# Kernel optimization log

Measured on AMD Instinct MI355X. Metric: run time of the kernel, lower is better.

Reference implementation:

```python
import jax, jax.numpy as jnp
import numpy as np

N_NODES = 50000
N_GENES = 512
N_EDGES = 800000
NUM_ITERATIONS = 5
MAX_CAP = 128
NNZ_FRAC = 0.1  # fraction of initially observed (nonzero) entries


def setup_inputs() -> dict:
    key = jax.random.key(0)
    k1, k2, k3, k4, k5 = jax.random.split(key, 5)
    x = jax.random.normal(k1, (N_NODES, N_GENES), dtype=jnp.float32)
    observed = jax.random.uniform(k2, (N_NODES, N_GENES)) < NNZ_FRAC
    x = jnp.where(observed, x, 0.0)  # sparse expression matrix
    edge_index = jax.random.randint(k3, (2, N_EDGES), 0, N_NODES, dtype=jnp.int32)
    edge_weight = jax.random.uniform(k4, (N_EDGES,), dtype=jnp.float32)
    max_imputation_per_cell = jax.random.randint(k5, (N_NODES,), 0, MAX_CAP, dtype=jnp.int32)
    return {
        "x": x,
        "edge_weight": edge_weight,
        "edge_index": edge_index,
        "max_imputation_per_cell": max_imputation_per_cell,
    }


def reference(x, edge_weight, edge_index, max_imputation_per_cell):
    n_nodes, n_genes = x.shape
    row, col = edge_index[0], edge_index[1]  # adj[row, col] = w; spmm: out[row] += w * x[col]
    original_x = x
    existing = x != 0  # observed entries are always reset to original values
    cap = max_imputation_per_cell[:, None]  # [N,1]
    base_key = jax.random.key(42)

    def step(carry, it):
        x, imp = carry
        # sparse adjacency propagation (torch.sparse.mm(adj, x))
        xp = jax.ops.segment_sum(edge_weight[:, None] * x[col], row, num_segments=n_nodes)
        # masked imputation reset: keep original observed values
        x = jnp.where(existing, original_x, xp)
        newly = (x != 0) & (~existing) & (~imp)
        imp = imp | newly
        # capacity-limited random reset: keep a random subset of at most
        # max_imputation_per_cell imputed genes per cell, zero the excess
        scores = jax.random.uniform(jax.random.fold_in(base_key, it), x.shape)
        scores = jnp.where(imp, scores, 2.0)  # non-imputed sort last (uniform < 1)
        rank = jnp.argsort(jnp.argsort(scores, axis=1), axis=1)  # rank among imputed
        keep = rank < cap
        reset = imp & (~keep)
        x = jnp.where(reset, 0.0, x)
        imp = imp & keep
        return (x, imp), None

    init = (x, jnp.zeros((n_nodes, n_genes), dtype=bool))
    (x, _), _ = jax.lax.scan(step, init, jnp.arange(NUM_ITERATIONS))
    return x
```

## Files before the change

### kernel.cpp

```cpp
#include <hip/hip_runtime.h>
#include <stdint.h>

#define N_NODES   50000
#define N_GENES   512
#define N_EDGES   800000
#define N_ITERS   5

#define C_CHUNKS  250
#define CHUNK_E   3200
#define NSUB      (CHUNK_E / 64)

#define REC_DW     384
#define REC_BYTES  1536

#define RECS_BYTES (50000ull * REC_BYTES + 256ull)
#define IMP_BYTES  3200000ull
#define CNT_BYTES  200000ull
#define PTR_BYTES  200004ull
#define CCOL_BYTES 3200000ull
#define CW_BYTES   3200000ull
#define RND_BYTES  50048ull
#define BSUM_BYTES 1024ull
#define WS_NEEDED (RECS_BYTES + IMP_BYTES + CNT_BYTES + PTR_BYTES + CCOL_BYTES + CW_BYTES + 2ull * RND_BYTES + BSUM_BYTES)

__host__ __device__ __forceinline__ uint32_t rotl32(uint32_t x, int r) {
  return (x << r) | (x >> (32 - r));
}

__host__ __device__ __forceinline__ void threefry2x32(uint32_t k0, uint32_t k1,
                                                      uint32_t x0, uint32_t x1,
                                                      uint32_t& o0, uint32_t& o1) {
  uint32_t k2 = k0 ^ k1 ^ 0x1BD11BDAu;
  x0 += k0; x1 += k1;
  x0 += x1; x1 = rotl32(x1, 13) ^ x0;
  x0 += x1; x1 = rotl32(x1, 15) ^ x0;
  x0 += x1; x1 = rotl32(x1, 26) ^ x0;
  x0 += x1; x1 = rotl32(x1, 6)  ^ x0;
  x0 += k1; x1 += k2 + 1u;
  x0 += x1; x1 = rotl32(x1, 17) ^ x0;
  x0 += x1; x1 = rotl32(x1, 29) ^ x0;
  x0 += x1; x1 = rotl32(x1, 16) ^ x0;
  x0 += x1; x1 = rotl32(x1, 24) ^ x0;
  x0 += k2; x1 += k0 + 2u;
  x0 += x1; x1 = rotl32(x1, 13) ^ x0;
  x0 += x1; x1 = rotl32(x1, 15) ^ x0;
  x0 += x1; x1 = rotl32(x1, 26) ^ x0;
  x0 += x1; x1 = rotl32(x1, 6)  ^ x0;
  x0 += k0; x1 += k1 + 3u;
  x0 += x1; x1 = rotl32(x1, 17) ^ x0;
  x0 += x1; x1 = rotl32(x1, 29) ^ x0;
  x0 += x1; x1 = rotl32(x1, 16) ^ x0;
  x0 += x1; x1 = rotl32(x1, 24) ^ x0;
  x0 += k1; x1 += k2 + 4u;
  x0 += x1; x1 = rotl32(x1, 13) ^ x0;
  x0 += x1; x1 = rotl32(x1, 15) ^ x0;
  x0 += x1; x1 = rotl32(x1, 26) ^ x0;
  x0 += x1; x1 = rotl32(x1, 6)  ^ x0;
  x0 += k2; x1 += k0 + 5u;
  o0 = x0; o1 = x1;
}

__device__ __forceinline__ uint32_t jax_bits_part32(uint32_t k0, uint32_t k1, uint32_t j) {
  uint32_t o0, o1;
  threefry2x32(k0, k1, 0u, j, o0, o1);
  return o0 ^ o1;
}

__global__ void chunk_hist(const int* __restrict__ rows, int* __restrict__ hist) {
  int c = blockIdx.x;
  int base = c * CHUNK_E;
  int* h = hist + (size_t)c * N_NODES;
  for (int i = threadIdx.x; i < CHUNK_E; i += blockDim.x)
    atomicAdd(&h[rows[base + i]], 1);
}

__global__ void row_scan(int* __restrict__ hist, int* __restrict__ cnt) {
  int r = blockIdx.x * blockDim.x + threadIdx.x;
  if (r >= N_NODES) return;
  int run = 0;
  for (int c = 0; c < C_CHUNKS; ++c) {
    size_t idx = (size_t)c * N_NODES + r;
    int t = hist[idx];
    hist[idx] = run;
    run += t;
  }
  cnt[r] = run;
}

#define SCAN_NB ((N_NODES + 255) / 256)
__global__ void scan_blk(const int* __restrict__ cnt, int* __restrict__ bsum) {
  int b = blockIdx.x, t = threadIdx.x;
  int i = b * 256 + t;
  int v = (i < N_NODES) ? cnt[i] : 0;
  int s = v;
  #pragma unroll
  for (int off = 32; off > 0; off >>= 1) s += __shfl_xor(s, off, 64);
  __shared__ int wsum[4];
  if ((t & 63) == 0) wsum[t >> 6] = s;
  __syncthreads();
  if (t == 0) bsum[b] = wsum[0] + wsum[1] + wsum[2] + wsum[3];
}

__global__ void scan_top(int* __restrict__ bsum) {
  int t = threadIdx.x;
  int lane = t & 63, wv = t >> 6;
  int v = (t < SCAN_NB) ? bsum[t] : 0;
  int incl = v;
  #pragma unroll
  for (int off = 1; off < 64; off <<= 1) {
    int u = __shfl_up(incl, off, 64);
    if (lane >= off) incl += u;
  }
  __shared__ int wtot[4];
  if (lane == 63) wtot[wv] = incl;
  __syncthreads();
  int woff = 0;
  for (int k = 0; k < 4; ++k) if (k < wv) woff += wtot[k];
  if (t < SCAN_NB) bsum[t] = woff + incl - v;
}

__global__ void scan_apply(const int* __restrict__ cnt, const int* __restrict__ bbase,
                           int* __restrict__ ptr) {
  int b = blockIdx.x, t = threadIdx.x;
  int i = b * 256 + t;
  int lane = t & 63, wv = t >> 6;
  int v = (i < N_NODES) ? cnt[i] : 0;
  int incl = v;
  #pragma unroll
  for (int off = 1; off < 64; off <<= 1) {
    int u = __shfl_up(incl, off, 64);
    if (lane >= off) incl += u;
  }
  __shared__ int wtot[4];
  if (lane == 63) wtot[wv] = incl;
  __syncthreads();
  int woff = bbase[b];
  for (int k = 0; k < 4; ++k) if (k < wv) woff += wtot[k];
  int excl = woff + incl - v;
  if (i < N_NODES) ptr[i] = excl;
  if (i == N_NODES - 1) ptr[N_NODES] = excl + v;
}

#define MATCH(RV, RANKV, CNTV, LASTV)                                     \
  { RANKV = 0; CNTV = 0; LASTV = 0;                                       \
    _Pragma("unroll 8")                                                   \
    for (int ii = 0; ii < 64; ++ii) {                                     \
      int ri_ = __shfl((RV), ii, 64);                                     \
      if (ri_ == (RV)) { CNTV++; if (ii < lane) RANKV++; LASTV = ii; }    \
    } }

__global__ __launch_bounds__(64) void scatter_par(
    const int* __restrict__ rows, const int* __restrict__ cols,
    const float* __restrict__ w, const int* __restrict__ ptr,
    int* __restrict__ hist, int* __restrict__ ccol, float* __restrict__ cw) {
  int c = blockIdx.x;
  int lane = threadIdx.x;
  int* h = hist + (size_t)c * N_NODES;
  int base = c * CHUNK_E;

  int rM = rows[base + lane], clM = cols[base + lane];
  float wvM = w[base + lane];
  int rankM, cntM, lastM;
  MATCH(rM, rankM, cntM, lastM)
  int rL = 0, clL = 0; float wvL = 0.f;
  if (NSUB > 1) {
    int e = base + 64 + lane;
    rL = rows[e]; clL = cols[e]; wvL = w[e];
  }
  for (int sub = 0; sub < NSUB; ++sub) {
    int oldM = 0;
    if (lane == lastM) oldM = atomicAdd(&h[rM], cntM);
    int rN = 0, clN = 0; float wvN = 0.f;
    if (sub + 2 < NSUB) {
      int e = base + (sub + 2) * 64 + lane;
      rN = rows[e]; clN = cols[e]; wvN = w[e];
    }
    int rankL = 0, cntL = 0, lastL = 0;
    if (sub + 1 < NSUB) { MATCH(rL, rankL, cntL, lastL) }
    int old = __shfl(oldM, lastM, 64);
    int pos = ptr[rM] + old + rankM;
    ccol[pos] = clM; cw[pos] = wvM;
    rM = rL; clM = clL; wvM = wvL; rankM = rankL; cntM = cntL; lastM = lastL;
    rL = rN; clL = clN; wvL = wvN;
  }
}

__device__ __forceinline__ void pack_row(uint32_t* __restrict__ rec,
                                         unsigned char* __restrict__ rnd_out,
                                         int lane, const float* rv) {
  uint32_t vm = 0;
  #pragma unroll
  for (int j = 0; j < 8; ++j) vm |= (rv[j] != 0.f) ? (1u << j) : 0u;
  int pF = __popc(vm & 15u);
  int pS = __popc(vm >> 4);
  int iF = pF, iS = pS;
  #pragma unroll
  for (int off = 1; off < 64; off <<= 1) {
    int uF = __shfl_up(iF, off, 64);
    int uS = __shfl_up(iS, off, 64);
    if (lane >= off) { iF += uF; iS += uS; }
  }
  int rF = iF - pF, rS = iS - pS;
  int tF = __shfl(iF, 63, 64);
  int tS = __shfl(iS, 63, 64);
  int b0 = tF + rS;
  float* vr = (float*)rec;
  ushort* gr = (ushort*)(rec + 256);
  int o = rF;
  #pragma unroll
  for (int j = 0; j < 4; ++j)
    if (vm & (1u << j)) {
      if (o < 256) { vr[o] = rv[j]; gr[o] = (ushort)((4 * lane + j) << 2); }
      o++;
    }
  o = b0;
  #pragma unroll
  for (int j = 4; j < 8; ++j)
    if (vm & (1u << j)) {
      if (o < 256) { vr[o] = rv[j]; gr[o] = (ushort)((256 + 4 * lane + (j - 4)) << 2); }
      o++;
    }
  int nz = min(tF + tS, 256);
  int rounds = max(1, (nz + 63) >> 6);
  int mpad = rounds << 6;
  int p = nz + lane;
  if (p < mpad) { vr[p] = 0.f; gr[p] = (ushort)(2048 + ((p & 63) << 2)); }
  if (lane == 63) *rnd_out = (unsigned char)rounds;
}

__global__ __launch_bounds__(256) void init_pack(const float* __restrict__ x,
                                                 uint32_t* __restrict__ recs,
                                                 unsigned char* __restrict__ rnd) {
  int wv = threadIdx.x >> 6, lane = threadIdx.x & 63;
  int r = blockIdx.x * 4 + wv;
  const float4* p4 = (const float4*)(x + (size_t)r * N_GENES);
  float4 pa = p4[lane], pb = p4[64 + lane];
  float rv[8] = {pa.x, pa.y, pa.z, pa.w, pb.x, pb.y, pb.z, pb.w};
  pack_row(recs + (size_t)r * REC_DW, rnd + r, lane, rv);
}

__device__ __forceinline__ int tr(uint32_t b) {
  return (int)(((b & 3u) << 6) | (b >> 2));
}

__device__ __forceinline__ float readlane_f(float v, int i) {
  return __int_as_float(__builtin_amdgcn_readlane(__float_as_int(v), i));
}

#define DECL_ST(S) int rd##S = 0; const uint32_t* rc##S = recs_p;         \
  float v0##S = 0.f, v1##S = 0.f, v2##S = 0.f;                            \
  int g0##S = 0, g1##S = 0, g2##S = 0;

#define ISSUE(S, IDX)                                                     \
  if ((IDX) < n) {                                                        \
    int cc_ = __builtin_amdgcn_readlane(cld, (IDX));                      \
    rd##S = __builtin_amdgcn_readlane(rdv, (IDX));                        \
    rc##S = recs_p + (size_t)cc_ * REC_DW;                                \
    const float* vr_ = (const float*)rc##S;                               \
    const ushort* gr_ = (const ushort*)(rc##S + 256);                     \
    v0##S = vr_[lane]; g0##S = gr_[lane];                                 \
    if (rd##S > 1) {                                                      \
      v1##S = vr_[64 + lane]; g1##S = gr_[64 + lane];                     \
      if (rd##S > 2) { v2##S = vr_[128 + lane]; g2##S = gr_[128 + lane]; }\
    }                                                                     \
  }

#define CONSUME(S, IDX)                                                   \
  { float wt_ = readlane_f(wld, (IDX));                                   \
    { float* p_ = (float*)((char*)accL + g0##S);                          \
      *p_ = *p_ + wt_ * v0##S; }                                          \
    if (rd##S > 1) {                                                      \
      { float* p_ = (float*)((char*)accL + g1##S);                        \
        *p_ = *p_ + wt_ * v1##S; }                                        \
      if (rd##S > 2) {                                                    \
        { float* p_ = (float*)((char*)accL + g2##S);                      \
          *p_ = *p_ + wt_ * v2##S; }                                      \
        if (rd##S > 3) {                                                  \
          float v3_ = ((const float*)rc##S)[192 + lane];                  \
          int g3_ = ((const ushort*)(rc##S + 256))[192 + lane];           \
          float* p_ = (float*)((char*)accL + g3_);                        \
          *p_ = *p_ + wt_ * v3_;                                          \
        }                                                                 \
      }                                                                   \
    } }

template <bool LAST>
__global__ __launch_bounds__(256) void prop_select(
    const uint32_t* __restrict__ recs_p, const unsigned char* __restrict__ rnd_p,
    const int* __restrict__ ptr, const int* __restrict__ ccol,
    const float* __restrict__ cw, unsigned char* __restrict__ imp,
    const int* __restrict__ cap_arr, uint32_t k0, uint32_t k1,
    uint32_t* __restrict__ recs_n, unsigned char* __restrict__ rnd_n,
    float* __restrict__ xdense) {
  #pragma clang fp contract(off)
  __shared__ int hist_s[4][256];
  __shared__ float accbuf[4][576];
  int wv = threadIdx.x >> 6;
  int lane = threadIdx.x & 63;
  int r = blockIdx.x * 4 + wv;
  int beg = ptr[r], end = ptr[r + 1];
  int* h = hist_s[wv];
  float* accL = accbuf[wv];

  unsigned char ibyte = imp[(size_t)r * 64 + lane];
  int cap = cap_arr[r];

  const float4 z4 = make_float4(0.f, 0.f, 0.f, 0.f);
  *(float4*)&accL[4 * lane] = z4;
  *(float4*)&accL[256 + 4 * lane] = z4;

  float pv[8];
  {
    int rdR = rnd_p[r];
    const float* vrR = (const float*)(recs_p + (size_t)r * REC_DW);
    const ushort* grR = (const ushort*)(recs_p + (size_t)r * REC_DW + 256);
    for (int t = 0; t < (rdR << 6); t += 64) {
      float v = vrR[t + lane];
      int g = grR[t + lane];
      *(float*)((char*)accL + g) = v;
    }
    float4 a = *(float4*)&accL[4 * lane];
    float4 b = *(float4*)&accL[256 + 4 * lane];
    pv[0] = a.x; pv[1] = a.y; pv[2] = a.z; pv[3] = a.w;
    pv[4] = b.x; pv[5] = b.y; pv[6] = b.z; pv[7] = b.w;
    *(float4*)&accL[4 * lane] = z4;
    *(float4*)&accL[256 + 4 * lane] = z4;
  }

  for (int base2 = beg; base2 < end; base2 += 64) {
    int n = min(64, end - base2);
    int cld = ccol[base2 + min(lane, n - 1)];
    float wld = (lane < n) ? cw[base2 + lane] : 0.f;
    int rdv = rnd_p[cld];

    DECL_ST(A) DECL_ST(B) DECL_ST(C) DECL_ST(D)
    ISSUE(A, 0) ISSUE(B, 1) ISSUE(C, 2) ISSUE(D, 3)
    int n4 = (n + 3) & ~3;
    for (int i = 0; i < n4; i += 4) {
      CONSUME(A, i)     ISSUE(A, i + 4)
      CONSUME(B, i + 1) ISSUE(B, i + 5)
      CONSUME(C, i + 2) ISSUE(C, i + 6)
      CONSUME(D, i + 3) ISSUE(D, i + 7)
    }
  }

  float4 aa = *(float4*)&accL[4 * lane];
  float4 ab = *(float4*)&accL[256 + 4 * lane];
  float acc[8] = {aa.x, aa.y, aa.z, aa.w, ab.x, ab.y, ab.z, ab.w};

  float val[8];
  bool ex[8];
  #pragma unroll
  for (int j = 0; j < 8; ++j) {
    ex[j] = (pv[j] != 0.f) && !((ibyte >> j) & 1);
    val[j] = ex[j] ? pv[j] : acc[j];
  }

  bool valid[8];
  int cnt_local = 0;
  #pragma unroll
  for (int j = 0; j < 8; ++j) {
    bool im = ((ibyte >> j) & 1) || ((val[j] != 0.f) && !ex[j]);
    valid[j] = im;
    cnt_local += im ? 1 : 0;
  }
  int nimp = cnt_local;
  #pragma unroll
  for (int off = 32; off > 0; off >>= 1) nimp += __shfl_xor(nimp, off, 64);

  bool keep_all = (nimp <= cap);
  bool keep_none = (!keep_all) && (cap <= 0);
  uint32_t key[8];
  uint32_t T = 0;
  bool use_T = false;

  if (!keep_all && !keep_none) {
    uint32_t goff = (uint32_t)r * (uint32_t)N_GENES;
    #pragma unroll
    for (int j = 0; j < 8; ++j) {
      int g = (j < 4) ? (4 * lane + j) : (256 + 4 * lane + (j - 4));
      uint32_t b = jax_bits_part32(k0, k1, goff + (uint32_t)g);
      key[j] = ((b >> 9) << 9) | (uint32_t)g;
    }
    h[lane] = 0; h[lane + 64] = 0; h[lane + 128] = 0; h[lane + 192] = 0;
    #pragma unroll
    for (int j = 0; j < 8; ++j)
      if (valid[j]) atomicAdd(&h[tr(key[j] >> 24)], 1);
    __threadfence_block();
    int c0 = h[lane], c1 = h[64 + lane], c2 = h[128 + lane], c3 = h[192 + lane];
    int lsum = c0 + c1 + c2 + c3;
    int incl = lsum;
    #pragma unroll
    for (int off = 1; off < 64; off <<= 1) {
      int v = __shfl_up(incl, off, 64);
      if (lane >= off) incl += v;
    }
    int excl = incl - lsum;
    int foundB = -1, foundRem = 0, cum = excl;
    if (cap > cum && cap <= cum + c0) { foundB = 4 * lane;     foundRem = cap - cum; } cum += c0;
    if (foundB < 0 && cap > cum && cap <= cum + c1) { foundB = 4 * lane + 1; foundRem = cap - cum; } cum += c1;
    if (foundB < 0 && cap > cum && cap <= cum + c2) { foundB = 4 * lane + 2; foundRem = cap - cum; } cum += c2;
    if (foundB < 0 && cap > cum && cap <= cum + c3) { foundB = 4 * lane + 3; foundRem = cap - cum; }
    unsigned long long mbal = __ballot(foundB >= 0);
    int src = __ffsll(mbal) - 1;
    int B   = __shfl(foundB, src, 64);
    int rem = __shfl(foundRem, src, 64);
    unsigned cm = 0;
    #pragma unroll
    for (int j = 0; j < 8; ++j)
      if (valid[j] && (int)(key[j] >> 24) == B) cm |= (1u << j);
    for (;;) {
      uint32_t m = 0xFFFFFFFFu;
      #pragma unroll
      for (int j = 0; j < 8; ++j)
        if (cm & (1u << j)) m = min(m, key[j]);
      #pragma unroll
      for (int off = 32; off > 0; off >>= 1)
        m = min(m, (uint32_t)__shfl_xor((int)m, off, 64));
      if (rem == 1) { T = m; break; }
      #pragma unroll
      for (int j = 0; j < 8; ++j)
        if ((cm & (1u << j)) && key[j] == m) cm &= ~(1u << j);
      rem--;
    }
    use_T = true;
  }

  float rv[8]; unsigned char ob8 = 0;
  #pragma unroll
  for (int j = 0; j < 8; ++j) {
    bool keep = valid[j] && (keep_all || (use_T && key[j] <= T));
    ob8 |= (unsigned char)(keep ? (1u << j) : 0u);
    rv[j] = (valid[j] && !keep) ? 0.f : val[j];
  }
  if (LAST) {
    float4* x4 = (float4*)(xdense + (size_t)r * N_GENES);
    x4[lane]      = make_float4(rv[0], rv[1], rv[2], rv[3]);
    x4[64 + lane] = make_float4(rv[4], rv[5], rv[6], rv[7]);
  } else {
    pack_row(recs_n + (size_t)r * REC_DW, rnd_n + r, lane, rv);
    imp[(size_t)r * 64 + lane] = ob8;
  }
}

__global__ void ws_probe(float* out, unsigned long long ws_bytes, unsigned long long needed) {
  if (ws_bytes < needed) out[0] = (float)ws_bytes;
}

extern "C" void kernel_launch(void* const* d_in, const int* in_sizes, int n_in,
                              void* d_out, int out_size, void* d_ws, size_t ws_size,
                              hipStream_t stream) {
  const float* x_in = (const float*)d_in[0];
  const float* ew   = (const float*)d_in[1];
  const int*   ei   = (const int*)d_in[2];
  const int*   cap  = (const int*)d_in[3];
  const int* rows = ei;
  const int* cols = ei + N_EDGES;
  float* out = (float*)d_out;

  char* ws = (char*)d_ws;
  uint32_t* recs_a = (uint32_t*)ws;         ws += RECS_BYTES;
  unsigned char* imp = (unsigned char*)ws;  ws += IMP_BYTES;
  int* cnt = (int*)ws;                      ws += CNT_BYTES;
  int* ptr = (int*)ws;                      ws += PTR_BYTES;
  int* ccol = (int*)ws;                     ws += CCOL_BYTES;
  float* cw = (float*)ws;                   ws += CW_BYTES;
  unsigned char* rnd_a = (unsigned char*)ws; ws += RND_BYTES;
  unsigned char* rnd_b = (unsigned char*)ws; ws += RND_BYTES;
  int* bsum = (int*)ws;                     ws += BSUM_BYTES;
  int* hist = (int*)d_ws;

  uint32_t* recs_b = (uint32_t*)d_out;

  hipMemsetAsync(hist, 0, (size_t)C_CHUNKS * N_NODES * sizeof(int), stream);
  hipMemsetAsync(imp, 0, IMP_BYTES, stream);

  chunk_hist<<<C_CHUNKS, 256, 0, stream>>>(rows, hist);
  row_scan<<<(N_NODES + 255) / 256, 256, 0, stream>>>(hist, cnt);
  scan_blk<<<SCAN_NB, 256, 0, stream>>>(cnt, bsum);
  scan_top<<<1, 256, 0, stream>>>(bsum);
  scan_apply<<<SCAN_NB, 256, 0, stream>>>(cnt, bsum, ptr);
  scatter_par<<<C_CHUNKS, 64, 0, stream>>>(rows, cols, ew, ptr, hist, ccol, cw);
  init_pack<<<N_NODES / 4, 256, 0, stream>>>(x_in, recs_a, rnd_a);

  uint32_t key_it[N_ITERS][2];
  for (int it = 0; it < N_ITERS; ++it) {
    uint32_t o0, o1;
    threefry2x32(0u, 42u, 0u, (uint32_t)it, o0, o1);
    key_it[it][0] = o0; key_it[it][1] = o1;
  }

  for (int it = 0; it < N_ITERS - 1; ++it) {
    bool a2b = (it & 1) == 0;
    prop_select<false><<<N_NODES / 4, 256, 0, stream>>>(
        a2b ? recs_a : recs_b, a2b ? rnd_a : rnd_b,
        ptr, ccol, cw, imp, cap, key_it[it][0], key_it[it][1],
        a2b ? recs_b : recs_a, a2b ? rnd_b : rnd_a, nullptr);
  }
  prop_select<true><<<N_NODES / 4, 256, 0, stream>>>(
      recs_a, rnd_a, ptr, ccol, cw, imp, cap,
      key_it[N_ITERS - 1][0], key_it[N_ITERS - 1][1],
      nullptr, nullptr, out);

  ws_probe<<<1, 1, 0, stream>>>(out, (unsigned long long)ws_size,
                                (unsigned long long)WS_NEEDED);
}
```

Baseline: 1.086 ms.

## Build chunk histograms in LDS, fuse scan kernels, deepen gather pipeline

Each chunk's histogram is now built in shared memory with packed 16-bit counters over two row-halves and written out densely. This removes the large histogram memset and the global atomics. row_scan is fused with the block-sum kernel, and the imp buffer is zeroed inside init_pack instead of by a separate memset. The neighbour-gather loop now keeps eight edges of loads in flight instead of four, with fewer prefetched rounds per edge, trading register pressure for memory-level parallelism.

```diff
diff --git a/kernel.cpp b/kernel.cpp
--- a/kernel.cpp
+++ b/kernel.cpp
@@ -66,41 +66,55 @@
   return o0 ^ o1;
 }
 
-__global__ void chunk_hist(const int* __restrict__ rows, int* __restrict__ hist) {
+#define HALF_R 25000
+__global__ __launch_bounds__(256) void chunk_hist(const int* __restrict__ rows,
+                                                  int* __restrict__ hist) {
+  __shared__ uint32_t lh[HALF_R / 2];
   int c = blockIdx.x;
   int base = c * CHUNK_E;
-  int* h = hist + (size_t)c * N_NODES;
-  for (int i = threadIdx.x; i < CHUNK_E; i += blockDim.x)
-    atomicAdd(&h[rows[base + i]], 1);
-}
-
-__global__ void row_scan(int* __restrict__ hist, int* __restrict__ cnt) {
+  for (int pass = 0; pass < 2; ++pass) {
+    int rlo = pass * HALF_R;
+    for (int i = threadIdx.x; i < HALF_R / 2; i += 256) lh[i] = 0;
+    __syncthreads();
+    for (int i = threadIdx.x; i < CHUNK_E; i += 256) {
+      int r = rows[base + i] - rlo;
+      if ((unsigned)r < (unsigned)HALF_R)
+        atomicAdd(&lh[r >> 1], 1u << ((r & 1) << 4));
+    }
+    __syncthreads();
+    int* out = hist + (size_t)c * N_NODES + rlo;
+    for (int i = threadIdx.x; i < HALF_R / 2; i += 256) {
+      uint32_t v = lh[i];
+      out[2 * i]     = (int)(v & 0xFFFFu);
+      out[2 * i + 1] = (int)(v >> 16);
+    }
+    __syncthreads();
+  }
+}
+
+__global__ void row_scan(int* __restrict__ hist, int* __restrict__ cnt,
+                         int* __restrict__ bsum) {
   int r = blockIdx.x * blockDim.x + threadIdx.x;
-  if (r >= N_NODES) return;
   int run = 0;
-  for (int c = 0; c < C_CHUNKS; ++c) {
-    size_t idx = (size_t)c * N_NODES + r;
-    int t = hist[idx];
-    hist[idx] = run;
-    run += t;
-  }
-  cnt[r] = run;
-}
-
-#define SCAN_NB ((N_NODES + 255) / 256)
-__global__ void scan_blk(const int* __restrict__ cnt, int* __restrict__ bsum) {
-  int b = blockIdx.x, t = threadIdx.x;
-  int i = b * 256 + t;
-  int v = (i < N_NODES) ? cnt[i] : 0;
-  int s = v;
+  if (r < N_NODES) {
+    for (int c = 0; c < C_CHUNKS; ++c) {
+      size_t idx = (size_t)c * N_NODES + r;
+      int t = hist[idx];
+      hist[idx] = run;
+      run += t;
+    }
+    cnt[r] = run;
+  }
+  int s = run;
   #pragma unroll
   for (int off = 32; off > 0; off >>= 1) s += __shfl_xor(s, off, 64);
   __shared__ int wsum[4];
-  if ((t & 63) == 0) wsum[t >> 6] = s;
+  if ((threadIdx.x & 63) == 0) wsum[threadIdx.x >> 6] = s;
   __syncthreads();
-  if (t == 0) bsum[b] = wsum[0] + wsum[1] + wsum[2] + wsum[3];
-}
-
+  if (threadIdx.x == 0) bsum[blockIdx.x] = wsum[0] + wsum[1] + wsum[2] + wsum[3];
+}
+
+#define SCAN_NB ((N_NODES + 255) / 256)
 __global__ void scan_top(int* __restrict__ bsum) {
   int t = threadIdx.x;
   int lane = t & 63, wv = t >> 6;
@@ -230,13 +244,15 @@
 
 __global__ __launch_bounds__(256) void init_pack(const float* __restrict__ x,
                                                  uint32_t* __restrict__ recs,
-                                                 unsigned char* __restrict__ rnd) {
+                                                 unsigned char* __restrict__ rnd,
+                                                 unsigned char* __restrict__ imp) {
   int wv = threadIdx.x >> 6, lane = threadIdx.x & 63;
   int r = blockIdx.x * 4 + wv;
   const float4* p4 = (const float4*)(x + (size_t)r * N_GENES);
   float4 pa = p4[lane], pb = p4[64 + lane];
   float rv[8] = {pa.x, pa.y, pa.z, pa.w, pb.x, pb.y, pb.z, pb.w};
   pack_row(recs + (size_t)r * REC_DW, rnd + r, lane, rv);
+  imp[(size_t)r * 64 + lane] = 0;
 }
 
 __device__ __forceinline__ int tr(uint32_t b) {
@@ -248,8 +264,8 @@
 }
 
 #define DECL_ST(S) int rd##S = 0; const uint32_t* rc##S = recs_p;         \
-  float v0##S = 0.f, v1##S = 0.f, v2##S = 0.f;                            \
-  int g0##S = 0, g1##S = 0, g2##S = 0;
+  float v0##S = 0.f, v1##S = 0.f;                                         \
+  int g0##S = 0, g1##S = 0;
 
 #define ISSUE(S, IDX)                                                     \
   if ((IDX) < n) {                                                        \
@@ -259,10 +275,7 @@
     const float* vr_ = (const float*)rc##S;                               \
     const ushort* gr_ = (const ushort*)(rc##S + 256);                     \
     v0##S = vr_[lane]; g0##S = gr_[lane];                                 \
-    if (rd##S > 1) {                                                      \
-      v1##S = vr_[64 + lane]; g1##S = gr_[64 + lane];                     \
-      if (rd##S > 2) { v2##S = vr_[128 + lane]; g2##S = gr_[128 + lane]; }\
-    }                                                                     \
+    if (rd##S > 1) { v1##S = vr_[64 + lane]; g1##S = gr_[64 + lane]; }    \
   }
 
 #define CONSUME(S, IDX)                                                   \
@@ -273,8 +286,10 @@
       { float* p_ = (float*)((char*)accL + g1##S);                        \
         *p_ = *p_ + wt_ * v1##S; }                                        \
       if (rd##S > 2) {                                                    \
-        { float* p_ = (float*)((char*)accL + g2##S);                      \
-          *p_ = *p_ + wt_ * v2##S; }                                      \
+        float v2_ = ((const float*)rc##S)[128 + lane];                    \
+        int g2_ = ((const ushort*)(rc##S + 256))[128 + lane];             \
+        { float* p_ = (float*)((char*)accL + g2_);                        \
+          *p_ = *p_ + wt_ * v2_; }                                        \
         if (rd##S > 3) {                                                  \
           float v3_ = ((const float*)rc##S)[192 + lane];                  \
           int g3_ = ((const ushort*)(rc##S + 256))[192 + lane];           \
@@ -334,13 +349,14 @@
     int rdv = rnd_p[cld];
 
     DECL_ST(A) DECL_ST(B) DECL_ST(C) DECL_ST(D)
+    DECL_ST(E) DECL_ST(F) DECL_ST(G) DECL_ST(H)
     ISSUE(A, 0) ISSUE(B, 1) ISSUE(C, 2) ISSUE(D, 3)
-    int n4 = (n + 3) & ~3;
-    for (int i = 0; i < n4; i += 4) {
-      CONSUME(A, i)     ISSUE(A, i + 4)
-      CONSUME(B, i + 1) ISSUE(B, i + 5)
-      CONSUME(C, i + 2) ISSUE(C, i + 6)
-      CONSUME(D, i + 3) ISSUE(D, i + 7)
+    int n8 = (n + 7) & ~7;
+    for (int i = 0; i < n8; i += 8) {
+      ISSUE(E, i + 4) ISSUE(F, i + 5) ISSUE(G, i + 6) ISSUE(H, i + 7)
+      CONSUME(A, i)     CONSUME(B, i + 1) CONSUME(C, i + 2) CONSUME(D, i + 3)
+      ISSUE(A, i + 8) ISSUE(B, i + 9) ISSUE(C, i + 10) ISSUE(D, i + 11)
+      CONSUME(E, i + 4) CONSUME(F, i + 5) CONSUME(G, i + 6) CONSUME(H, i + 7)
     }
   }
 
@@ -472,16 +488,12 @@
 
   uint32_t* recs_b = (uint32_t*)d_out;
 
-  hipMemsetAsync(hist, 0, (size_t)C_CHUNKS * N_NODES * sizeof(int), stream);
-  hipMemsetAsync(imp, 0, IMP_BYTES, stream);
-
   chunk_hist<<<C_CHUNKS, 256, 0, stream>>>(rows, hist);
-  row_scan<<<(N_NODES + 255) / 256, 256, 0, stream>>>(hist, cnt);
-  scan_blk<<<SCAN_NB, 256, 0, stream>>>(cnt, bsum);
+  row_scan<<<SCAN_NB, 256, 0, stream>>>(hist, cnt, bsum);
   scan_top<<<1, 256, 0, stream>>>(bsum);
   scan_apply<<<SCAN_NB, 256, 0, stream>>>(cnt, bsum, ptr);
   scatter_par<<<C_CHUNKS, 64, 0, stream>>>(rows, cols, ew, ptr, hist, ccol, cw);
-  init_pack<<<N_NODES / 4, 256, 0, stream>>>(x_in, recs_a, rnd_a);
+  init_pack<<<N_NODES / 4, 256, 0, stream>>>(x_in, recs_a, rnd_a, imp);
 
   uint32_t key_it[N_ITERS][2];
   for (int it = 0; it < N_ITERS; ++it) {
```

Result: slower. 1.189 ms (+9.5%).
